# Performance work log

Measured on AMD Instinct MI355X. Metric: run time of the kernel, lower is better.

Reference implementation:

```python
import jax, jax.numpy as jnp
import numpy as np

EPS = 1e-6

def setup_inputs() -> dict:
    key = jax.random.key(0)
    ks = jax.random.split(key, 9)
    B, D, F = 8192, 2048, 1024
    s_in = 1.0 / np.sqrt(D)
    return {
        "Q": jax.random.normal(ks[0], (B, D), jnp.float32),
        "K": jax.random.normal(ks[1], (B, D), jnp.float32),
        "V": jax.random.normal(ks[2], (B, D), jnp.float32),
        "Wq": jax.random.normal(ks[3], (D, F), jnp.float32) * s_in,
        "bq": jnp.zeros((F,), jnp.float32),
        "Wk": jax.random.normal(ks[4], (D, F), jnp.float32) * s_in,
        "bk": jnp.zeros((F,), jnp.float32),
        "Wv": jax.random.normal(ks[5], (D, D), jnp.float32) * s_in,
        "bv": jnp.zeros((D,), jnp.float32),
    }

def reference(Q, K, V, Wq, bq, Wk, bk, Wv, bv):
    # feature maps: Linear + ELU (note: ELU, no +1, matching the source)
    Q_feat = jax.nn.elu(Q @ Wq + bq)          # (B, F)
    K_feat = jax.nn.elu(K @ Wk + bk)          # (B, F)
    V_proj = V @ Wv + bv                      # (B, D)
    # torch: KV = outer(K_feat, V_proj); QKV = Q_feat @ KV
    # equivalent without materializing (B, F, D):
    qk = jnp.einsum('bi,bi->b', Q_feat, K_feat)      # (B,)
    QKV = qk[:, None] * V_proj                        # (B, D)
    # Z = 1 / (sum_i Q_feat * sum_i K_feat + eps)
    Z = 1.0 / (Q_feat.sum(-1) * K_feat.sum(-1) + EPS)  # (B,)
    return QKV * Z[:, None]
```

## Files before the change

### kernel.cpp

```cpp
#include <hip/hip_runtime.h>
#include <hip/hip_fp16.h>
#include <cstdint>
#include <cstddef>

typedef _Float16 f16x8 __attribute__((ext_vector_type(8)));
typedef _Float16 f16x4 __attribute__((ext_vector_type(4)));
typedef float    f32x4 __attribute__((ext_vector_type(4)));

#define GPTR(p) ((const __attribute__((address_space(1))) void*)(p))
#define SPTR(p) ((__attribute__((address_space(3))) void*)(p))

__global__ void transpose_cast_kernel(const float* __restrict__ W,
                                      _Float16* __restrict__ Wt,
                                      int R, int C) {
  __shared__ float tile[32][33];
  const int c  = blockIdx.x * 32 + threadIdx.x;
  const int r0 = blockIdx.y * 32;
  for (int i = threadIdx.y; i < 32; i += 8)
    tile[i][threadIdx.x] = W[(size_t)(r0 + i) * C + c];
  __syncthreads();
  const int out_c = r0 + threadIdx.x;
  const int oc0   = blockIdx.x * 32;
  for (int i = threadIdx.y; i < 32; i += 8)
    Wt[(size_t)(oc0 + i) * R + out_c] = (_Float16)tile[threadIdx.x][i];
}

__global__ void cast_f32_f16_kernel(const float* __restrict__ src,
                                    _Float16* __restrict__ dst) {
  const size_t i = (size_t)blockIdx.x * 256 + threadIdx.x;
  const float4 v = ((const float4*)src)[i];
  f16x4 h;
  h[0] = (_Float16)v.x; h[1] = (_Float16)v.y;
  h[2] = (_Float16)v.z; h[3] = (_Float16)v.w;
  ((f16x4*)dst)[i] = h;
}

#define STG8(kk, h, slotv) do {                                                \
    __builtin_amdgcn_global_load_lds(GPTR(aRow + (h) * hstep + (kk)),          \
        SPTR(Aring + (slotv) * 4096 + wave * 512), 16, 0, 0);                  \
    __builtin_amdgcn_global_load_lds(GPTR(bRow + (h) * hstep + (kk)),          \
        SPTR(Bring + (slotv) * 4096 + wave * 512), 16, 0, 0);                  \
  } while (0)

#define WINDOW8(t_, DOSTG, DOWAIT, VCSTR) do {                                 \
    const int e_ = (2 * (t_)) & 7;                                             \
    const _Float16* Ab_ = Aring + ((e_ + wm) & 7) * 4096;                      \
    const _Float16* Bb_ = Bring + ((e_ + (wn >> 1)) & 7) * 4096                \
                          + (wn & 1) * 2048;                                   \
    f16x8 bf_[4], afL_[4], afH_[4];                                            \
    _Pragma("unroll")                                                          \
    for (int j_ = 0; j_ < 4; ++j_)                                             \
      bf_[j_] = *(const f16x8*)(Bb_ + j_ * 512 + lane_c * 8);                  \
    _Pragma("unroll")                                                          \
    for (int i_ = 0; i_ < 4; ++i_)                                             \
      afL_[i_] = *(const f16x8*)(Ab_ + i_ * 512 + lane_c * 8);                 \
    _Pragma("unroll")                                                          \
    for (int i_ = 0; i_ < 4; ++i_)                                             \
      afH_[i_] = *(const f16x8*)(Ab_ + (i_ + 4) * 512 + lane_c * 8);           \
    __builtin_amdgcn_s_setprio(1);                                             \
    _Pragma("unroll")                                                          \
    for (int i_ = 0; i_ < 4; ++i_)                                             \
      _Pragma("unroll")                                                        \
      for (int j_ = 0; j_ < 4; ++j_)                                           \
        acc[i_][j_] = __builtin_amdgcn_mfma_f32_16x16x32_f16(afL_[i_], bf_[j_],\
                                                             acc[i_][j_],      \
                                                             0, 0, 0);         \
    if (DOSTG) {                                                               \
      STG8(((t_) + 3) * 32, 0, (e_ + 6) & 7);                                  \
      STG8(((t_) + 3) * 32, 1, (e_ + 7) & 7);                                  \
    }                                                                          \
    _Pragma("unroll")                                                          \
    for (int i_ = 0; i_ < 4; ++i_)                                             \
      _Pragma("unroll")                                                        \
      for (int j_ = 0; j_ < 4; ++j_)                                           \
        acc[i_ + 4][j_] = __builtin_amdgcn_mfma_f32_16x16x32_f16(afH_[i_],     \
                                                                 bf_[j_],      \
                                                                 acc[i_ + 4][j_],\
                                                                 0, 0, 0);     \
    __builtin_amdgcn_s_setprio(0);                                             \
    if (DOWAIT) asm volatile("s_waitcnt vmcnt(" VCSTR ")" ::: "memory");       \
    __builtin_amdgcn_s_barrier();                                              \
    asm volatile("" ::: "memory");                                             \
  } while (0)

template <int MODE, bool OUTHALF>
__global__ __launch_bounds__(512, 2) void gemm8p(
    const _Float16* __restrict__ A,
    const _Float16* __restrict__ Bt0, const _Float16* __restrict__ Bt1,
    const float* __restrict__ bias0, const float* __restrict__ bias1,
    int msplit, const float* __restrict__ scale,
    void* __restrict__ Cv, int K, int N) {
  __shared__ __align__(16) _Float16 Aring[8 * 4096];
  __shared__ __align__(16) _Float16 Bring[8 * 4096];

  const int tid  = threadIdx.x;
  const int lane = tid & 63;
  const int wave = tid >> 6;
  const int quad = lane >> 4;
  const int r    = lane & 15;
  const int wm   = wave >> 2;
  const int wn   = wave & 3;

  const int gx  = gridDim.x;
  const int nwg = gx * gridDim.y;
  int flat = blockIdx.y * gx + blockIdx.x;
  if ((nwg & 7) == 0) flat = (flat & 7) * (nwg >> 3) + (flat >> 3);
  const int m0 = (flat / gx) * 256;
  const int n0 = (flat % gx) * 256;

  const _Float16* Bt   = (m0 >= msplit) ? Bt1 : Bt0;
  const float*    bias = (m0 >= msplit) ? bias1 : bias0;

  const int sp  = tid >> 3;
  const int sub = (tid & 7) ^ (sp & 7);
  const int lr  = sp * 2 + (sub >> 2);
  const int sc  = sub & 3;
  const _Float16* aRow = A  + (size_t)(m0 + lr) * K + sc * 8;
  const _Float16* bRow = Bt + (size_t)(n0 + lr) * K + sc * 8;
  const int hstep = 128 * K;

  const int lane_c = (r >> 1) * 8 + (((((r & 1) << 2) | quad)) ^ (r >> 1));

  f32x4 acc[8][4] = {};
  const int NT = K >> 5;

#pragma unroll
  for (int tt = 0; tt < 3; ++tt) {
    STG8(tt * 32, 0, (2 * tt) & 7);
    STG8(tt * 32, 1, (2 * tt + 1) & 7);
  }
  asm volatile("s_waitcnt vmcnt(8)" ::: "memory");
  __builtin_amdgcn_s_barrier();
  asm volatile("" ::: "memory");

  for (int t = 0; t < NT - 3; ++t) WINDOW8(t, 1, 1, "8");
  WINDOW8(NT - 3, 0, 1, "4");
  WINDOW8(NT - 2, 0, 1, "0");
  WINDOW8(NT - 1, 0, 0, "0");

  float*    Cf = (float*)Cv;
  _Float16* Ch = (_Float16*)Cv;
#pragma unroll
  for (int i = 0; i < 8; ++i) {
    const int row0 = m0 + wm * 128 + i * 16 + quad * 4;
#pragma unroll
    for (int j = 0; j < 4; ++j) {
      const int col = n0 + wn * 64 + j * 16 + r;
      const float b = bias[col];
#pragma unroll
      for (int reg = 0; reg < 4; ++reg) {
        const int row = row0 + reg;
        float v = acc[i][j][reg] + b;
        if (MODE == 0) v = v > 0.f ? v : (expf(v) - 1.f);
        else           v = v * scale[row];
        if (OUTHALF) Ch[(size_t)row * N + col] = (_Float16)v;
        else         Cf[(size_t)row * N + col] = v;
      }
    }
  }
}

#undef STG8
#undef WINDOW8

template <int MODE, bool AHALF, bool OUTHALF>
__global__ __launch_bounds__(256) void gemm2(
    const void* __restrict__ Av,
    const _Float16* __restrict__ Bt0, const _Float16* __restrict__ Bt1,
    const float* __restrict__ bias0, const float* __restrict__ bias1,
    int msplit, const float* __restrict__ scale,
    void* __restrict__ Cv, int K, int N) {
  constexpr int BK = 64;
  __shared__ __align__(16) _Float16 As[128 * BK];
  __shared__ __align__(16) _Float16 Bs[128 * BK];

  const int tid  = threadIdx.x;
  const int lane = tid & 63;
  const int wave = tid >> 6;
  const int quad = lane >> 4;
  const int r    = lane & 15;
  const int wm   = wave >> 1;
  const int wn   = wave & 1;
  const int m0   = blockIdx.y * 128;
  const int n0   = blockIdx.x * 128;

  const _Float16* Bt  = (m0 >= msplit) ? Bt1 : Bt0;
  const float* bias   = (m0 >= msplit) ? bias1 : bias0;

  size_t aoff[4], boff[4];
  int slot[4];
#pragma unroll
  for (int t = 0; t < 4; ++t) {
    const int s  = wave * 256 + t * 64 + lane;
    const int n  = s >> 3;
    const int kc = (s & 7) ^ (n & 7);
    aoff[t] = (size_t)(m0 + n) * K + kc * 8;
    boff[t] = (size_t)(n0 + n) * K + kc * 8;
    slot[t] = s;
  }

  f32x4 acc[4][4] = {};
  const _Float16* Ah = (const _Float16*)Av;
  const float*    Af = (const float*)Av;

  for (int k0 = 0; k0 < K; k0 += BK) {
    __syncthreads();
    if (AHALF) {
#pragma unroll
      for (int t = 0; t < 4; ++t)
        __builtin_amdgcn_global_load_lds(GPTR(Ah + aoff[t] + k0),
                                         SPTR(As + (wave * 256 + t * 64) * 8),
                                         16, 0, 0);
    } else {
#pragma unroll
      for (int t = 0; t < 4; ++t) {
        const float* ap = Af + aoff[t] + k0;
        const float4 v0 = *(const float4*)ap;
        const float4 v1 = *(const float4*)(ap + 4);
        f16x8 h;
        h[0] = (_Float16)v0.x; h[1] = (_Float16)v0.y;
        h[2] = (_Float16)v0.z; h[3] = (_Float16)v0.w;
        h[4] = (_Float16)v1.x; h[5] = (_Float16)v1.y;
        h[6] = (_Float16)v1.z; h[7] = (_Float16)v1.w;
        *(f16x8*)(As + (size_t)slot[t] * 8) = h;
      }
    }
#pragma unroll
    for (int t = 0; t < 4; ++t)
      __builtin_amdgcn_global_load_lds(GPTR(Bt + boff[t] + k0),
                                       SPTR(Bs + (wave * 256 + t * 64) * 8),
                                       16, 0, 0);
    __syncthreads();

#pragma unroll
    for (int ki = 0; ki < 2; ++ki) {
      f16x8 af[4], bf[4];
#pragma unroll
      for (int i = 0; i < 4; ++i) {
        const int an = wm * 64 + i * 16 + r;
        af[i] = *(const f16x8*)(As + (an * 8 + ((ki * 4 + quad) ^ (an & 7))) * 8);
      }
#pragma unroll
      for (int j = 0; j < 4; ++j) {
        const int bn = wn * 64 + j * 16 + r;
        bf[j] = *(const f16x8*)(Bs + (bn * 8 + ((ki * 4 + quad) ^ (bn & 7))) * 8);
      }
#pragma unroll
      for (int i = 0; i < 4; ++i)
#pragma unroll
        for (int j = 0; j < 4; ++j)
          acc[i][j] = __builtin_amdgcn_mfma_f32_16x16x32_f16(af[i], bf[j],
                                                             acc[i][j], 0, 0, 0);
    }
  }

  float*    Cf = (float*)Cv;
  _Float16* Ch = (_Float16*)Cv;
#pragma unroll
  for (int i = 0; i < 4; ++i) {
#pragma unroll
    for (int j = 0; j < 4; ++j) {
      const int col = n0 + wn * 64 + j * 16 + r;
      const float b = bias[col];
#pragma unroll
      for (int reg = 0; reg < 4; ++reg) {
        const int row = m0 + wm * 64 + i * 16 + quad * 4 + reg;
        float v = acc[i][j][reg] + b;
        if (MODE == 0) v = v > 0.f ? v : (expf(v) - 1.f);
        else           v = v * scale[row];
        if (OUTHALF) Ch[(size_t)row * N + col] = (_Float16)v;
        else         Cf[(size_t)row * N + col] = v;
      }
    }
  }
}

template <bool HALF>
__global__ void reduce_scale2(const void* __restrict__ Qf,
                              const void* __restrict__ Kf,
                              float* __restrict__ scale) {
  const int b = blockIdx.x;
  const int t = threadIdx.x;
  float q[4], k[4];
  if (HALF) {
    const f16x4 qh = ((const f16x4*)((const _Float16*)Qf + (size_t)b * 1024))[t];
    const f16x4 kh = ((const f16x4*)((const _Float16*)Kf + (size_t)b * 1024))[t];
#pragma unroll
    for (int i = 0; i < 4; ++i) { q[i] = (float)qh[i]; k[i] = (float)kh[i]; }
  } else {
    const float4 qv = ((const float4*)((const float*)Qf + (size_t)b * 1024))[t];
    const float4 kv = ((const float4*)((const float*)Kf + (size_t)b * 1024))[t];
    q[0] = qv.x; q[1] = qv.y; q[2] = qv.z; q[3] = qv.w;
    k[0] = kv.x; k[1] = kv.y; k[2] = kv.z; k[3] = kv.w;
  }
  float qk = q[0] * k[0] + q[1] * k[1] + q[2] * k[2] + q[3] * k[3];
  float sq = q[0] + q[1] + q[2] + q[3];
  float sk = k[0] + k[1] + k[2] + k[3];
#pragma unroll
  for (int off = 32; off > 0; off >>= 1) {
    qk += __shfl_down(qk, off, 64);
    sq += __shfl_down(sq, off, 64);
    sk += __shfl_down(sk, off, 64);
  }
  __shared__ float buf[3][4];
  const int lane = t & 63, wv = t >> 6;
  if (lane == 0) { buf[0][wv] = qk; buf[1][wv] = sq; buf[2][wv] = sk; }
  __syncthreads();
  if (t == 0) {
    const float QK = buf[0][0] + buf[0][1] + buf[0][2] + buf[0][3];
    const float SQ = buf[1][0] + buf[1][1] + buf[1][2] + buf[1][3];
    const float SK = buf[2][0] + buf[2][1] + buf[2][2] + buf[2][3];
    scale[b] = QK / (SQ * SK + 1e-6f);
  }
}

extern "C" void kernel_launch(void* const* d_in, const int* in_sizes, int n_in,
                              void* d_out, int out_size, void* d_ws,
                              size_t ws_size, hipStream_t stream) {
  const float* Q  = (const float*)d_in[0];
  const float* K_ = (const float*)d_in[1];
  const float* V  = (const float*)d_in[2];
  const float* Wq = (const float*)d_in[3];
  const float* bq = (const float*)d_in[4];
  const float* Wk = (const float*)d_in[5];
  const float* bk = (const float*)d_in[6];
  const float* Wv = (const float*)d_in[7];
  const float* bv = (const float*)d_in[8];
  float* out = (float*)d_out;

  const int B = 8192, D = 2048, F = 1024;
  const size_t MiB = 1u << 20;
  char* ws = (char*)d_ws;

  const size_t NEED_FAST = 40 * MiB + 64 * 1024;

  if (ws_size >= NEED_FAST) {
    _Float16* WqT = (_Float16*)ws;
    _Float16* WkT = (_Float16*)(ws + 4 * MiB);
    _Float16* WvT = (_Float16*)ws;
    _Float16* QfH = (_Float16*)(ws + 8 * MiB);
    _Float16* KfH = (_Float16*)(ws + 24 * MiB);
    _Float16* Vh  = (_Float16*)(ws + 8 * MiB);
    float* scale  = (float*)(ws + 40 * MiB);
    _Float16* Qh = (_Float16*)d_out;
    _Float16* Kh = (_Float16*)d_out + (size_t)B * D;

    dim3 tb(32, 8);
    transpose_cast_kernel<<<dim3(F / 32, D / 32), tb, 0, stream>>>(Wq, WqT, D, F);
    transpose_cast_kernel<<<dim3(F / 32, D / 32), tb, 0, stream>>>(Wk, WkT, D, F);
    const int castBlocks = (B * D / 4) / 256;
    cast_f32_f16_kernel<<<castBlocks, 256, 0, stream>>>(Q,  Qh);
    cast_f32_f16_kernel<<<castBlocks, 256, 0, stream>>>(K_, Kh);

    gemm8p<0, true><<<dim3(F / 256, (2 * B) / 256), 512, 0, stream>>>(
        Qh, WqT, WkT, bq, bk, B, nullptr, QfH, D, F);
    reduce_scale2<true><<<B, 256, 0, stream>>>(QfH, KfH, scale);

    cast_f32_f16_kernel<<<castBlocks, 256, 0, stream>>>(V, Vh);
    transpose_cast_kernel<<<dim3(D / 32, D / 32), tb, 0, stream>>>(Wv, WvT, D, D);
    gemm8p<1, false><<<dim3(D / 256, B / 256), 512, 0, stream>>>(
        Vh, WvT, WvT, bv, bv, 1 << 30, scale, out, D, D);
  } else {
    _Float16* WqT = (_Float16*)ws;
    _Float16* WkT = (_Float16*)(ws + 4 * MiB);
    _Float16* WvT = (_Float16*)(ws + 8 * MiB);
    float* scale  = (float*)(ws + 16 * MiB);
    float* Qf = out;
    float* Kf = out + (size_t)B * F;

    dim3 tb(32, 8);
    transpose_cast_kernel<<<dim3(F / 32, D / 32), tb, 0, stream>>>(Wq, WqT, D, F);
    transpose_cast_kernel<<<dim3(F / 32, D / 32), tb, 0, stream>>>(Wk, WkT, D, F);
    transpose_cast_kernel<<<dim3(D / 32, D / 32), tb, 0, stream>>>(Wv, WvT, D, D);

    gemm2<0, false, false><<<dim3(F / 128, B / 128), 256, 0, stream>>>(
        Q, WqT, WqT, bq, bq, 1 << 30, nullptr, Qf, D, F);
    gemm2<0, false, false><<<dim3(F / 128, B / 128), 256, 0, stream>>>(
        K_, WkT, WkT, bk, bk, 1 << 30, nullptr, Kf, D, F);
    reduce_scale2<false><<<B, 256, 0, stream>>>(Qf, Kf, scale);
    gemm2<1, false, false><<<dim3(D / 128, B / 128), 256, 0, stream>>>(
        V, WvT, WvT, bv, bv, 1 << 30, scale, out, D, D);
  }
}
```

Baseline: 394.5 us.

## Split GEMM window into two barrier phases and merge prep kernels

Each k-window of the fp16 MFMA GEMM is split into two half-phases, each with its own barrier. The global-to-LDS stage and the LDS fragment loads for the high half are interleaved between the two MFMA batches rather than issued all together. The aim is to overlap LDS reads and global prefetch with matrix work and to spread memory traffic more evenly, at the cost of an extra barrier per window. Separately, the Wq/Wk transposes and the Q/K casts are each merged into one launch to cut launch overhead.

```diff
diff --git a/kernel.cpp b/kernel.cpp
--- a/kernel.cpp
+++ b/kernel.cpp
@@ -25,6 +25,25 @@
     Wt[(size_t)(oc0 + i) * R + out_c] = (_Float16)tile[threadIdx.x][i];
 }
 
+__global__ void transpose_cast2_kernel(const float* __restrict__ W0,
+                                       _Float16* __restrict__ Wt0,
+                                       const float* __restrict__ W1,
+                                       _Float16* __restrict__ Wt1,
+                                       int R, int C) {
+  const float* __restrict__ W  = blockIdx.z ? W1  : W0;
+  _Float16*    __restrict__ Wt = blockIdx.z ? Wt1 : Wt0;
+  __shared__ float tile[32][33];
+  const int c  = blockIdx.x * 32 + threadIdx.x;
+  const int r0 = blockIdx.y * 32;
+  for (int i = threadIdx.y; i < 32; i += 8)
+    tile[i][threadIdx.x] = W[(size_t)(r0 + i) * C + c];
+  __syncthreads();
+  const int out_c = r0 + threadIdx.x;
+  const int oc0   = blockIdx.x * 32;
+  for (int i = threadIdx.y; i < 32; i += 8)
+    Wt[(size_t)(oc0 + i) * R + out_c] = (_Float16)tile[threadIdx.x][i];
+}
+
 __global__ void cast_f32_f16_kernel(const float* __restrict__ src,
                                     _Float16* __restrict__ dst) {
   const size_t i = (size_t)blockIdx.x * 256 + threadIdx.x;
@@ -35,6 +54,18 @@
   ((f16x4*)dst)[i] = h;
 }
 
+__global__ void cast2_f32_f16_kernel(const float* __restrict__ s0,
+                                     const float* __restrict__ s1,
+                                     _Float16* __restrict__ dst, int half4) {
+  const int i = blockIdx.x * 256 + threadIdx.x;
+  const float4 v = (i < half4) ? ((const float4*)s0)[i]
+                               : ((const float4*)s1)[i - half4];
+  f16x4 h;
+  h[0] = (_Float16)v.x; h[1] = (_Float16)v.y;
+  h[2] = (_Float16)v.z; h[3] = (_Float16)v.w;
+  ((f16x4*)dst)[i] = h;
+}
+
 #define STG8(kk, h, slotv) do {                                                \
     __builtin_amdgcn_global_load_lds(GPTR(aRow + (h) * hstep + (kk)),          \
         SPTR(Aring + (slotv) * 4096 + wave * 512), 16, 0, 0);                  \
@@ -48,15 +79,16 @@
     const _Float16* Bb_ = Bring + ((e_ + (wn >> 1)) & 7) * 4096                \
                           + (wn & 1) * 2048;                                   \
     f16x8 bf_[4], afL_[4], afH_[4];                                            \
+                 \
     _Pragma("unroll")                                                          \
     for (int j_ = 0; j_ < 4; ++j_)                                             \
       bf_[j_] = *(const f16x8*)(Bb_ + j_ * 512 + lane_c * 8);                  \
     _Pragma("unroll")                                                          \
     for (int i_ = 0; i_ < 4; ++i_)                                             \
       afL_[i_] = *(const f16x8*)(Ab_ + i_ * 512 + lane_c * 8);                 \
-    _Pragma("unroll")                                                          \
-    for (int i_ = 0; i_ < 4; ++i_)                                             \
-      afH_[i_] = *(const f16x8*)(Ab_ + (i_ + 4) * 512 + lane_c * 8);           \
+    if (DOSTG) STG8(((t_) + 3) * 32, 0, (e_ + 6) & 7);                         \
+    __builtin_amdgcn_s_barrier();                                              \
+    asm volatile("" ::: "memory");                                             \
     __builtin_amdgcn_s_setprio(1);                                             \
     _Pragma("unroll")                                                          \
     for (int i_ = 0; i_ < 4; ++i_)                                             \
@@ -65,10 +97,16 @@
         acc[i_][j_] = __builtin_amdgcn_mfma_f32_16x16x32_f16(afL_[i_], bf_[j_],\
                                                              acc[i_][j_],      \
                                                              0, 0, 0);         \
-    if (DOSTG) {                                                               \
-      STG8(((t_) + 3) * 32, 0, (e_ + 6) & 7);                                  \
-      STG8(((t_) + 3) * 32, 1, (e_ + 7) & 7);                                  \
-    }                                                                          \
+    __builtin_amdgcn_s_setprio(0);                                             \
+               \
+    _Pragma("unroll")                                                          \
+    for (int i_ = 0; i_ < 4; ++i_)                                             \
+      afH_[i_] = *(const f16x8*)(Ab_ + (i_ + 4) * 512 + lane_c * 8);           \
+    if (DOSTG) STG8(((t_) + 3) * 32, 1, (e_ + 7) & 7);                         \
+    if (DOWAIT) asm volatile("s_waitcnt vmcnt(" VCSTR ")" ::: "memory");       \
+    __builtin_amdgcn_s_barrier();                                              \
+    asm volatile("" ::: "memory");                                             \
+    __builtin_amdgcn_s_setprio(1);                                             \
     _Pragma("unroll")                                                          \
     for (int i_ = 0; i_ < 4; ++i_)                                             \
       _Pragma("unroll")                                                        \
@@ -78,9 +116,6 @@
                                                                  acc[i_ + 4][j_],\
                                                                  0, 0, 0);     \
     __builtin_amdgcn_s_setprio(0);                                             \
-    if (DOWAIT) asm volatile("s_waitcnt vmcnt(" VCSTR ")" ::: "memory");       \
-    __builtin_amdgcn_s_barrier();                                              \
-    asm volatile("" ::: "memory");                                             \
   } while (0)
 
 template <int MODE, bool OUTHALF>
@@ -346,17 +381,16 @@
     _Float16* Kh = (_Float16*)d_out + (size_t)B * D;
 
     dim3 tb(32, 8);
-    transpose_cast_kernel<<<dim3(F / 32, D / 32), tb, 0, stream>>>(Wq, WqT, D, F);
-    transpose_cast_kernel<<<dim3(F / 32, D / 32), tb, 0, stream>>>(Wk, WkT, D, F);
-    const int castBlocks = (B * D / 4) / 256;
-    cast_f32_f16_kernel<<<castBlocks, 256, 0, stream>>>(Q,  Qh);
-    cast_f32_f16_kernel<<<castBlocks, 256, 0, stream>>>(K_, Kh);
+    transpose_cast2_kernel<<<dim3(F / 32, D / 32, 2), tb, 0, stream>>>(
+        Wq, WqT, Wk, WkT, D, F);
+    const int half4 = B * D / 4;
+    cast2_f32_f16_kernel<<<2 * half4 / 256, 256, 0, stream>>>(Q, K_, Qh, half4);
 
     gemm8p<0, true><<<dim3(F / 256, (2 * B) / 256), 512, 0, stream>>>(
         Qh, WqT, WkT, bq, bk, B, nullptr, QfH, D, F);
     reduce_scale2<true><<<B, 256, 0, stream>>>(QfH, KfH, scale);
 
-    cast_f32_f16_kernel<<<castBlocks, 256, 0, stream>>>(V, Vh);
+    cast_f32_f16_kernel<<<half4 / 256, 256, 0, stream>>>(V, Vh);
     transpose_cast_kernel<<<dim3(D / 32, D / 32), tb, 0, stream>>>(Wv, WvT, D, D);
     gemm8p<1, false><<<dim3(D / 256, B / 256), 512, 0, stream>>>(
         Vh, WvT, WvT, bv, bv, 1 << 30, scale, out, D, D);
```

Result: no change. 393.3 us (-0.3%).

## Fuse prep and mid launches and split GEMM window into two barrier phases

Applied to the files above, without the earlier changes.

The weight transpose-casts and the Q/K casts are merged into one prep kernel. The row reduction, the Wv transpose and the V cast are merged into one mid kernel, which needs a larger workspace so Vh no longer aliases QfH. Inside the GEMM main loop, each window is split into two half-phases, each with its own LDS read, global-to-LDS stage and barrier, to interleave loads with MFMA work. This cuts launch count and tail gaps, at the cost of an extra barrier per window and a dependence on workspace size for the merged path.

```diff
diff --git a/kernel.cpp b/kernel.cpp
--- a/kernel.cpp
+++ b/kernel.cpp
@@ -35,6 +35,92 @@
   ((f16x4*)dst)[i] = h;
 }
 
+__global__ __launch_bounds__(256) void prep_kernel(
+    const float* __restrict__ Wq, _Float16* __restrict__ WqT,
+    const float* __restrict__ Wk, _Float16* __restrict__ WkT,
+    const float* __restrict__ Q,  const float* __restrict__ K_,
+    _Float16* __restrict__ QKh) {
+  const int b = blockIdx.x;
+  if (b < 4096) {
+    const float* __restrict__ W  = (b < 2048) ? Wq : Wk;
+    _Float16*    __restrict__ Wt = (b < 2048) ? WqT : WkT;
+    const int bb = b & 2047;
+    const int bx = bb & 31;
+    const int by = bb >> 5;
+    __shared__ float tile[32][33];
+    const int tx = threadIdx.x & 31, ty = threadIdx.x >> 5;
+    const int c = bx * 32 + tx, r0 = by * 32;
+    for (int i = ty; i < 32; i += 8)
+      tile[i][tx] = W[(size_t)(r0 + i) * 1024 + c];
+    __syncthreads();
+    const int out_c = r0 + tx, oc0 = bx * 32;
+    for (int i = ty; i < 32; i += 8)
+      Wt[(size_t)(oc0 + i) * 2048 + out_c] = (_Float16)tile[tx][i];
+  } else {
+    const int half4 = 8192 * 2048 / 4;
+    const int i = (b - 4096) * 256 + (int)threadIdx.x;
+    const float4 v = (i < half4) ? ((const float4*)Q)[i]
+                                 : ((const float4*)K_)[i - half4];
+    f16x4 h;
+    h[0] = (_Float16)v.x; h[1] = (_Float16)v.y;
+    h[2] = (_Float16)v.z; h[3] = (_Float16)v.w;
+    ((f16x4*)QKh)[i] = h;
+  }
+}
+
+__global__ __launch_bounds__(256) void mid_kernel(
+    const _Float16* __restrict__ QfH, const _Float16* __restrict__ KfH,
+    float* __restrict__ scale,
+    const float* __restrict__ Wv, _Float16* __restrict__ WvT,
+    const float* __restrict__ V, _Float16* __restrict__ Vh) {
+  const int b = blockIdx.x;
+  if (b < 2048) {
+    const int wv = threadIdx.x >> 6, lane = threadIdx.x & 63;
+    const int row = b * 4 + wv;
+    const _Float16* qrow = QfH + (size_t)row * 1024;
+    const _Float16* krow = KfH + (size_t)row * 1024;
+    const f16x8 q0 = ((const f16x8*)qrow)[lane * 2];
+    const f16x8 q1 = ((const f16x8*)qrow)[lane * 2 + 1];
+    const f16x8 k0 = ((const f16x8*)krow)[lane * 2];
+    const f16x8 k1 = ((const f16x8*)krow)[lane * 2 + 1];
+    float qk = 0.f, sq = 0.f, sk = 0.f;
+#pragma unroll
+    for (int i = 0; i < 8; ++i) {
+      float q = (float)q0[i], k = (float)k0[i];
+      qk += q * k; sq += q; sk += k;
+      q = (float)q1[i]; k = (float)k1[i];
+      qk += q * k; sq += q; sk += k;
+    }
+#pragma unroll
+    for (int off = 32; off > 0; off >>= 1) {
+      qk += __shfl_down(qk, off, 64);
+      sq += __shfl_down(sq, off, 64);
+      sk += __shfl_down(sk, off, 64);
+    }
+    if (lane == 0) scale[row] = qk / (sq * sk + 1e-6f);
+  } else if (b < 6144) {
+    const int bb = b - 2048;
+    const int bx = bb & 63;
+    const int by = bb >> 6;
+    __shared__ float tile[32][33];
+    const int tx = threadIdx.x & 31, ty = threadIdx.x >> 5;
+    const int c = bx * 32 + tx, r0 = by * 32;
+    for (int i = ty; i < 32; i += 8)
+      tile[i][tx] = Wv[(size_t)(r0 + i) * 2048 + c];
+    __syncthreads();
+    const int out_c = r0 + tx, oc0 = bx * 32;
+    for (int i = ty; i < 32; i += 8)
+      WvT[(size_t)(oc0 + i) * 2048 + out_c] = (_Float16)tile[tx][i];
+  } else {
+    const int i = (b - 6144) * 256 + (int)threadIdx.x;
+    const float4 v = ((const float4*)V)[i];
+    f16x4 h;
+    h[0] = (_Float16)v.x; h[1] = (_Float16)v.y;
+    h[2] = (_Float16)v.z; h[3] = (_Float16)v.w;
+    ((f16x4*)Vh)[i] = h;
+  }
+}
+
 #define STG8(kk, h, slotv) do {                                                \
     __builtin_amdgcn_global_load_lds(GPTR(aRow + (h) * hstep + (kk)),          \
         SPTR(Aring + (slotv) * 4096 + wave * 512), 16, 0, 0);                  \
@@ -48,15 +134,16 @@
     const _Float16* Bb_ = Bring + ((e_ + (wn >> 1)) & 7) * 4096                \
                           + (wn & 1) * 2048;                                   \
     f16x8 bf_[4], afL_[4], afH_[4];                                            \
+                 \
     _Pragma("unroll")                                                          \
     for (int j_ = 0; j_ < 4; ++j_)                                             \
       bf_[j_] = *(const f16x8*)(Bb_ + j_ * 512 + lane_c * 8);                  \
     _Pragma("unroll")                                                          \
     for (int i_ = 0; i_ < 4; ++i_)                                             \
       afL_[i_] = *(const f16x8*)(Ab_ + i_ * 512 + lane_c * 8);                 \
-    _Pragma("unroll")                                                          \
-    for (int i_ = 0; i_ < 4; ++i_)                                             \
-      afH_[i_] = *(const f16x8*)(Ab_ + (i_ + 4) * 512 + lane_c * 8);           \
+    if (DOSTG) STG8(((t_) + 3) * 32, 0, (e_ + 6) & 7);                         \
+    __builtin_amdgcn_s_barrier();                                              \
+    asm volatile("" ::: "memory");                                             \
     __builtin_amdgcn_s_setprio(1);                                             \
     _Pragma("unroll")                                                          \
     for (int i_ = 0; i_ < 4; ++i_)                                             \
@@ -65,10 +152,16 @@
         acc[i_][j_] = __builtin_amdgcn_mfma_f32_16x16x32_f16(afL_[i_], bf_[j_],\
                                                              acc[i_][j_],      \
                                                              0, 0, 0);         \
-    if (DOSTG) {                                                               \
-      STG8(((t_) + 3) * 32, 0, (e_ + 6) & 7);                                  \
-      STG8(((t_) + 3) * 32, 1, (e_ + 7) & 7);                                  \
-    }                                                                          \
+    __builtin_amdgcn_s_setprio(0);                                             \
+               \
+    _Pragma("unroll")                                                          \
+    for (int i_ = 0; i_ < 4; ++i_)                                             \
+      afH_[i_] = *(const f16x8*)(Ab_ + (i_ + 4) * 512 + lane_c * 8);           \
+    if (DOSTG) STG8(((t_) + 3) * 32, 1, (e_ + 7) & 7);                         \
+    if (DOWAIT) asm volatile("s_waitcnt vmcnt(" VCSTR ")" ::: "memory");       \
+    __builtin_amdgcn_s_barrier();                                              \
+    asm volatile("" ::: "memory");                                             \
+    __builtin_amdgcn_s_setprio(1);                                             \
     _Pragma("unroll")                                                          \
     for (int i_ = 0; i_ < 4; ++i_)                                             \
       _Pragma("unroll")                                                        \
@@ -78,9 +171,6 @@
                                                                  acc[i_ + 4][j_],\
                                                                  0, 0, 0);     \
     __builtin_amdgcn_s_setprio(0);                                             \
-    if (DOWAIT) asm volatile("s_waitcnt vmcnt(" VCSTR ")" ::: "memory");       \
-    __builtin_amdgcn_s_barrier();                                              \
-    asm volatile("" ::: "memory");                                             \
   } while (0)
 
 template <int MODE, bool OUTHALF>
@@ -332,7 +422,8 @@
   const size_t MiB = 1u << 20;
   char* ws = (char*)d_ws;
 
-  const size_t NEED_FAST = 40 * MiB + 64 * 1024;
+  const size_t NEED_FAST  = 40 * MiB + 64 * 1024;
+  const size_t NEED_FAST2 = 73 * MiB;
 
   if (ws_size >= NEED_FAST) {
     _Float16* WqT = (_Float16*)ws;
@@ -340,24 +431,26 @@
     _Float16* WvT = (_Float16*)ws;
     _Float16* QfH = (_Float16*)(ws + 8 * MiB);
     _Float16* KfH = (_Float16*)(ws + 24 * MiB);
-    _Float16* Vh  = (_Float16*)(ws + 8 * MiB);
     float* scale  = (float*)(ws + 40 * MiB);
+    const bool merged = (ws_size >= NEED_FAST2);
+    _Float16* Vh = merged ? (_Float16*)(ws + 41 * MiB)
+                          : (_Float16*)(ws + 8 * MiB);
     _Float16* Qh = (_Float16*)d_out;
     _Float16* Kh = (_Float16*)d_out + (size_t)B * D;
-
-    dim3 tb(32, 8);
-    transpose_cast_kernel<<<dim3(F / 32, D / 32), tb, 0, stream>>>(Wq, WqT, D, F);
-    transpose_cast_kernel<<<dim3(F / 32, D / 32), tb, 0, stream>>>(Wk, WkT, D, F);
-    const int castBlocks = (B * D / 4) / 256;
-    cast_f32_f16_kernel<<<castBlocks, 256, 0, stream>>>(Q,  Qh);
-    cast_f32_f16_kernel<<<castBlocks, 256, 0, stream>>>(K_, Kh);
+    (void)Kh;
+
+    prep_kernel<<<36864, 256, 0, stream>>>(Wq, WqT, Wk, WkT, Q, K_, Qh);
 
     gemm8p<0, true><<<dim3(F / 256, (2 * B) / 256), 512, 0, stream>>>(
         Qh, WqT, WkT, bq, bk, B, nullptr, QfH, D, F);
-    reduce_scale2<true><<<B, 256, 0, stream>>>(QfH, KfH, scale);
-
-    cast_f32_f16_kernel<<<castBlocks, 256, 0, stream>>>(V, Vh);
-    transpose_cast_kernel<<<dim3(D / 32, D / 32), tb, 0, stream>>>(Wv, WvT, D, D);
+
+    if (merged) {
+      mid_kernel<<<22528, 256, 0, stream>>>(QfH, KfH, scale, Wv, WvT, V, Vh);
+    } else {
+      mid_kernel<<<6144, 256, 0, stream>>>(QfH, KfH, scale, Wv, WvT, V, Vh);
+      cast_f32_f16_kernel<<<(B * D / 4) / 256, 256, 0, stream>>>(V, Vh);
+    }
+
     gemm8p<1, false><<<dim3(D / 256, B / 256), 512, 0, stream>>>(
         Vh, WvT, WvT, bv, bv, 1 << 30, scale, out, D, D);
   } else {
```

Measured after the change: 379.4 us. -3.8%, faster.
